# Kernel optimization log

Hardware: AMD Instinct MI355X
Metric: run time of the kernel (lower is better)

## Reference

```python
import jax, jax.numpy as jnp
import numpy as np

ALIGN_WEIGHT = 1.0
UNIFORM_WEIGHT = 1.0
ALIGN_ALPHA = 2.0
UNIFORM_T = 2.0
EPS = 1e-12  # F.normalize eps


def setup_inputs() -> dict:
    key = jax.random.key(0)
    ka, kb = jax.random.split(key)
    B, D = 4096, 256
    return {
        "embeddings_a": jax.random.normal(ka, (B, D), dtype=jnp.float32),
        "embeddings_b": jax.random.normal(kb, (B, D), dtype=jnp.float32),
    }


def _l2_normalize(x):
    # matches F.normalize(p=2, dim=1): x / max(||x||, eps)
    n = jnp.sqrt(jnp.sum(x * x, axis=1, keepdims=True))
    return x / jnp.maximum(n, EPS)


def reference(embeddings_a, embeddings_b):
    a = _l2_normalize(embeddings_a)
    b = _l2_normalize(embeddings_b)

    # alignment: mean ||a_i - b_i||^alpha (alpha=2 -> squared euclidean)
    diff = a - b
    dist = jnp.sqrt(jnp.sum(diff * diff, axis=1))
    align_loss = jnp.mean(dist ** ALIGN_ALPHA)

    # uniformity over concatenated views: mean over strict upper triangle of
    # exp(-t * d_ij^2). Matrix is symmetric with exp(0)=1 on the diagonal, so
    # mean_{i<j} = (sum_all - n) / (n*(n-1)). d^2 = 2 - 2<x_i, x_j> on sphere.
    x = jnp.concatenate([a, b], axis=0)  # [n, d]
    n = x.shape[0]
    gram = x @ x.T                        # [n, n]
    sq = jnp.sum(x * x, axis=1)           # [n]
    d2 = jnp.maximum(sq[:, None] + sq[None, :] - 2.0 * gram, 0.0)
    e = jnp.exp(-UNIFORM_T * d2)
    uniform_loss = (jnp.sum(e) - n) / (n * (n - 1))

    return ALIGN_WEIGHT * align_loss + UNIFORM_WEIGHT * uniform_loss
```

## Files before the change

### kernel.cpp

```cpp
#include <hip/hip_runtime.h>
#include <math.h>

#define D_DIM 256

typedef __attribute__((ext_vector_type(8))) short short8v;
typedef __attribute__((ext_vector_type(16))) float f32x16;

#define AS_GLOBAL(p) ((const __attribute__((address_space(1))) void*)(p))
#define AS_LDS(p)    ((__attribute__((address_space(3))) void*)(p))

__device__ __forceinline__ unsigned short f2bf(float f) {
    unsigned int u = __float_as_uint(f);
    unsigned int r = (u + 0x7fffu + ((u >> 16) & 1u)) >> 16;
    return (unsigned short)r;
}

__global__ __launch_bounds__(256) void normalize_kernel(
        const float* __restrict__ A, const float* __restrict__ Bm,
        unsigned short* __restrict__ Xb, float* __restrict__ SQ,
        float* __restrict__ partials, int B_rows) {
    __shared__ float red[4];
    int lane = threadIdx.x & 63;
    int w    = threadIdx.x >> 6;
    int i    = blockIdx.x * 4 + w;

    const float4* A4 = (const float4*)(A + (size_t)i * D_DIM);
    const float4* B4 = (const float4*)(Bm + (size_t)i * D_DIM);
    float4 av = A4[lane];
    float4 bv = B4[lane];

    float sa = av.x*av.x + av.y*av.y + av.z*av.z + av.w*av.w;
    float sb = bv.x*bv.x + bv.y*bv.y + bv.z*bv.z + bv.w*bv.w;
    #pragma unroll
    for (int off = 32; off > 0; off >>= 1) {
        sa += __shfl_xor(sa, off, 64);
        sb += __shfl_xor(sb, off, 64);
    }
    float dena = fmaxf(sqrtf(sa), 1e-12f);
    float denb = fmaxf(sqrtf(sb), 1e-12f);
    float ia = 1.0f / dena, ib = 1.0f / denb;

    float4 an = {av.x*ia, av.y*ia, av.z*ia, av.w*ia};
    float4 bn = {bv.x*ib, bv.y*ib, bv.z*ib, bv.w*ib};

    ushort4 ua = {f2bf(an.x), f2bf(an.y), f2bf(an.z), f2bf(an.w)};
    ushort4 ub = {f2bf(bn.x), f2bf(bn.y), f2bf(bn.z), f2bf(bn.w)};
    ((ushort4*)(Xb + (size_t)i * D_DIM))[lane]            = ua;
    ((ushort4*)(Xb + (size_t)(B_rows + i) * D_DIM))[lane] = ub;

    float dx = an.x-bn.x, dy = an.y-bn.y, dz = an.z-bn.z, dw = an.w-bn.w;
    float sd = dx*dx + dy*dy + dz*dz + dw*dw;
    #pragma unroll
    for (int off = 32; off > 0; off >>= 1) sd += __shfl_down(sd, off, 64);

    if (lane == 0) {
        SQ[i]          = sa * ia * ia;
        SQ[B_rows + i] = sb * ib * ib;
        red[w] = sd;
    }
    __syncthreads();
    if (threadIdx.x == 0)
        atomicAdd(&partials[blockIdx.x & 63], red[0]+red[1]+red[2]+red[3]);
}

__device__ __forceinline__ short8v frag_read(const unsigned short* base, int r, int kb) {
    int off = r * 128 + (kb ^ ((r & 7) << 4));
    return *reinterpret_cast<const short8v*>(reinterpret_cast<const char*>(base) + off);
}

__global__ __launch_bounds__(256) void uniform_mfma_kernel(
        const unsigned short* __restrict__ Xb, const float* __restrict__ SQ,
        float* __restrict__ partials) {
    int ib = blockIdx.x, jb = blockIdx.y;
    if (jb < ib) return;

    __shared__ __align__(16) unsigned short As[128 * 64];
    __shared__ __align__(16) unsigned short Bs[128 * 64];
    __shared__ float sqa[128], sqb[128], red[4];

    int t    = threadIdx.x;
    int lane = t & 63;
    int w    = t >> 6;
    int wr   = w >> 1, wc = w & 1;

    int rowA0 = ib * 128, rowB0 = jb * 128;
    if (t < 128) sqa[t] = SQ[rowA0 + t];
    else         sqb[t - 128] = SQ[rowB0 + t - 128];

    f32x16 acc[2][2] = {};

    int r_a0 = wr * 64 + (lane & 31), r_a1 = r_a0 + 32;
    int r_b0 = wc * 64 + (lane & 31), r_b1 = r_b0 + 32;

    for (int k0 = 0; k0 < D_DIM; k0 += 64) {
        __syncthreads();
        #pragma unroll
        for (int it = 0; it < 4; ++it) {
            int row   = w * 32 + it * 8 + (lane >> 3);
            int chunk = ((lane & 7) ^ ((lane >> 3) & 7)) << 3;
            const unsigned short* srcA = Xb + (size_t)(rowA0 + row) * D_DIM + k0 + chunk;
            const unsigned short* srcB = Xb + (size_t)(rowB0 + row) * D_DIM + k0 + chunk;
            unsigned short* dA = As + (w * 32 + it * 8) * 64;
            unsigned short* dB = Bs + (w * 32 + it * 8) * 64;
            __builtin_amdgcn_global_load_lds(AS_GLOBAL(srcA), AS_LDS(dA), 16, 0, 0);
            __builtin_amdgcn_global_load_lds(AS_GLOBAL(srcB), AS_LDS(dB), 16, 0, 0);
        }
        __syncthreads();

        #pragma unroll
        for (int kk = 0; kk < 4; ++kk) {
            int kb = kk * 32 + ((lane >> 5) << 4);
            short8v a0 = frag_read(As, r_a0, kb);
            short8v a1 = frag_read(As, r_a1, kb);
            short8v b0 = frag_read(Bs, r_b0, kb);
            short8v b1 = frag_read(Bs, r_b1, kb);
            acc[0][0] = __builtin_amdgcn_mfma_f32_32x32x16_bf16(a0, b0, acc[0][0], 0, 0, 0);
            acc[0][1] = __builtin_amdgcn_mfma_f32_32x32x16_bf16(a0, b1, acc[0][1], 0, 0, 0);
            acc[1][0] = __builtin_amdgcn_mfma_f32_32x32x16_bf16(a1, b0, acc[1][0], 0, 0, 0);
            acc[1][1] = __builtin_amdgcn_mfma_f32_32x32x16_bf16(a1, b1, acc[1][1], 0, 0, 0);
        }
    }

    float s = 0.0f;
    int col = lane & 31;
    int rhi = (lane >> 5) * 4;
    #pragma unroll
    for (int si = 0; si < 2; ++si)
        #pragma unroll
        for (int sj = 0; sj < 2; ++sj)
            #pragma unroll
            for (int reg = 0; reg < 16; ++reg) {
                int il = wr * 64 + si * 32 + (reg & 3) + 8 * (reg >> 2) + rhi;
                int jl = wc * 64 + sj * 32 + col;
                float d2 = fmaxf(sqa[il] + sqb[jl] - 2.0f * acc[si][sj][reg], 0.0f);
                s += __expf(-2.0f * d2);
            }
    if (ib != jb) s *= 2.0f;

    #pragma unroll
    for (int off = 32; off > 0; off >>= 1) s += __shfl_down(s, off, 64);
    if (lane == 0) red[w] = s;
    __syncthreads();
    if (t == 0)
        atomicAdd(&partials[64 + ((ib * 7 + jb * 13) & 63)], red[0]+red[1]+red[2]+red[3]);
}

__global__ void finalize_kernel(const float* __restrict__ partials,
                                float* __restrict__ out, int B_rows) {
    int t = threadIdx.x;
    float al = partials[t];
    float un = partials[64 + t];
    #pragma unroll
    for (int off = 32; off > 0; off >>= 1) {
        al += __shfl_down(al, off, 64);
        un += __shfl_down(un, off, 64);
    }
    if (t == 0) {
        float n = (float)(2 * B_rows);
        out[0] = al / (float)B_rows + (un - n) / (n * (n - 1.0f));
    }
}

extern "C" void kernel_launch(void* const* d_in, const int* in_sizes, int n_in,
                              void* d_out, int out_size, void* d_ws, size_t ws_size,
                              hipStream_t stream) {
    const float* A  = (const float*)d_in[0];
    const float* Bm = (const float*)d_in[1];
    float* out = (float*)d_out;

    int B_rows = in_sizes[0] / D_DIM;
    int n_tot  = 2 * B_rows;

    unsigned short* Xb = (unsigned short*)d_ws;
    float* SQ       = (float*)(Xb + (size_t)n_tot * D_DIM);
    float* partials = SQ + n_tot;

    hipMemsetAsync(partials, 0, 128 * sizeof(float), stream);

    normalize_kernel<<<B_rows / 4, 256, 0, stream>>>(A, Bm, Xb, SQ, partials, B_rows);

    int nb = n_tot / 128;
    uniform_mfma_kernel<<<dim3(nb, nb), 256, 0, stream>>>(Xb, SQ, partials);

    finalize_kernel<<<1, 64, 0, stream>>>(partials, out, B_rows);
}
```

Baseline: 98.38 us.

## Launch triangular grid, switch to 16x16x32 MFMA, drop atomics and memset

```diff
diff --git a/kernel.cpp b/kernel.cpp
--- a/kernel.cpp
+++ b/kernel.cpp
@@ -2,9 +2,12 @@
 #include <math.h>
 
 #define D_DIM 256
+#define TILE  128
+#define BKE   64
+#define LDS_PAD 3072
 
 typedef __attribute__((ext_vector_type(8))) short short8v;
-typedef __attribute__((ext_vector_type(16))) float f32x16;
+typedef __attribute__((ext_vector_type(4))) float f32x4;
 
 #define AS_GLOBAL(p) ((const __attribute__((address_space(1))) void*)(p))
 #define AS_LDS(p)    ((__attribute__((address_space(3))) void*)(p))
@@ -60,79 +63,84 @@
     }
     __syncthreads();
     if (threadIdx.x == 0)
-        atomicAdd(&partials[blockIdx.x & 63], red[0]+red[1]+red[2]+red[3]);
-}
-
-__device__ __forceinline__ short8v frag_read(const unsigned short* base, int r, int kb) {
+        partials[blockIdx.x] = red[0]+red[1]+red[2]+red[3];
+}
+
+__device__ __forceinline__ short8v frag_read(const short* base, int r, int kb) {
     int off = r * 128 + (kb ^ ((r & 7) << 4));
     return *reinterpret_cast<const short8v*>(reinterpret_cast<const char*>(base) + off);
 }
 
-__global__ __launch_bounds__(256) void uniform_mfma_kernel(
+__global__ __launch_bounds__(256, 3) void uniform_mfma_kernel(
         const unsigned short* __restrict__ Xb, const float* __restrict__ SQ,
-        float* __restrict__ partials) {
-    int ib = blockIdx.x, jb = blockIdx.y;
-    if (jb < ib) return;
-
-    __shared__ __align__(16) unsigned short As[128 * 64];
-    __shared__ __align__(16) unsigned short Bs[128 * 64];
-    __shared__ float sqa[128], sqb[128], red[4];
+        float* __restrict__ partials, int n_panels) {
+    __shared__ __align__(16) short As[TILE * BKE + LDS_PAD];
+    __shared__ __align__(16) short Bs[TILE * BKE + LDS_PAD];
+    __shared__ float sqa[TILE], sqb[TILE], red[4];
 
     int t    = threadIdx.x;
     int lane = t & 63;
     int w    = t >> 6;
-    int wr   = w >> 1, wc = w & 1;
-
-    int rowA0 = ib * 128, rowB0 = jb * 128;
-    if (t < 128) sqa[t] = SQ[rowA0 + t];
-    else         sqb[t - 128] = SQ[rowB0 + t - 128];
-
-    f32x16 acc[2][2] = {};
-
-    int r_a0 = wr * 64 + (lane & 31), r_a1 = r_a0 + 32;
-    int r_b0 = wc * 64 + (lane & 31), r_b1 = r_b0 + 32;
-
-    for (int k0 = 0; k0 < D_DIM; k0 += 64) {
+    int wr   = w >> 1;
+    int wc   = w & 1;
+
+    int rem = blockIdx.x;
+    int ib  = 0;
+    while (rem >= n_panels - ib) { rem -= n_panels - ib; ++ib; }
+    int jb = ib + rem;
+
+    int rowA0 = ib * TILE, rowB0 = jb * TILE;
+    if (t < TILE) sqa[t]        = SQ[rowA0 + t];
+    else          sqb[t - TILE] = SQ[rowB0 + t - TILE];
+
+    f32x4 acc[4][4] = {};
+
+    for (int k0 = 0; k0 < D_DIM; k0 += BKE) {
         __syncthreads();
         #pragma unroll
         for (int it = 0; it < 4; ++it) {
-            int row   = w * 32 + it * 8 + (lane >> 3);
-            int chunk = ((lane & 7) ^ ((lane >> 3) & 7)) << 3;
-            const unsigned short* srcA = Xb + (size_t)(rowA0 + row) * D_DIM + k0 + chunk;
-            const unsigned short* srcB = Xb + (size_t)(rowB0 + row) * D_DIM + k0 + chunk;
-            unsigned short* dA = As + (w * 32 + it * 8) * 64;
-            unsigned short* dB = Bs + (w * 32 + it * 8) * 64;
-            __builtin_amdgcn_global_load_lds(AS_GLOBAL(srcA), AS_LDS(dA), 16, 0, 0);
-            __builtin_amdgcn_global_load_lds(AS_GLOBAL(srcB), AS_LDS(dB), 16, 0, 0);
+            int row  = w * 32 + it * 8 + (lane >> 3);
+            int gel  = (((lane & 7) ^ (row & 7)) << 3);
+            const unsigned short* sA = Xb + (size_t)(rowA0 + row) * D_DIM + k0 + gel;
+            const unsigned short* sB = Xb + (size_t)(rowB0 + row) * D_DIM + k0 + gel;
+            short* dA = As + (w * 32 + it * 8) * BKE;
+            short* dB = Bs + (w * 32 + it * 8) * BKE;
+            __builtin_amdgcn_global_load_lds(AS_GLOBAL(sA), AS_LDS(dA), 16, 0, 0);
+            __builtin_amdgcn_global_load_lds(AS_GLOBAL(sB), AS_LDS(dB), 16, 0, 0);
         }
         __syncthreads();
 
         #pragma unroll
-        for (int kk = 0; kk < 4; ++kk) {
-            int kb = kk * 32 + ((lane >> 5) << 4);
-            short8v a0 = frag_read(As, r_a0, kb);
-            short8v a1 = frag_read(As, r_a1, kb);
-            short8v b0 = frag_read(Bs, r_b0, kb);
-            short8v b1 = frag_read(Bs, r_b1, kb);
-            acc[0][0] = __builtin_amdgcn_mfma_f32_32x32x16_bf16(a0, b0, acc[0][0], 0, 0, 0);
-            acc[0][1] = __builtin_amdgcn_mfma_f32_32x32x16_bf16(a0, b1, acc[0][1], 0, 0, 0);
-            acc[1][0] = __builtin_amdgcn_mfma_f32_32x32x16_bf16(a1, b0, acc[1][0], 0, 0, 0);
-            acc[1][1] = __builtin_amdgcn_mfma_f32_32x32x16_bf16(a1, b1, acc[1][1], 0, 0, 0);
+        for (int kk = 0; kk < 2; ++kk) {
+            int kb = kk * 64 + ((lane >> 4) << 4);
+            short8v a[4], b[4];
+            #pragma unroll
+            for (int m = 0; m < 4; ++m)
+                a[m] = frag_read(As, wr * 64 + m * 16 + (lane & 15), kb);
+            #pragma unroll
+            for (int n = 0; n < 4; ++n)
+                b[n] = frag_read(Bs, wc * 64 + n * 16 + (lane & 15), kb);
+            #pragma unroll
+            for (int m = 0; m < 4; ++m)
+                #pragma unroll
+                for (int n = 0; n < 4; ++n)
+                    acc[m][n] = __builtin_amdgcn_mfma_f32_16x16x32_bf16(
+                        a[m], b[n], acc[m][n], 0, 0, 0);
         }
     }
 
-    float s = 0.0f;
-    int col = lane & 31;
-    int rhi = (lane >> 5) * 4;
-    #pragma unroll
-    for (int si = 0; si < 2; ++si)
+    float s   = 0.0f;
+    int   col = lane & 15;
+    int   rhi = (lane >> 4) * 4;
+    #pragma unroll
+    for (int m = 0; m < 4; ++m)
         #pragma unroll
-        for (int sj = 0; sj < 2; ++sj)
-            #pragma unroll
-            for (int reg = 0; reg < 16; ++reg) {
-                int il = wr * 64 + si * 32 + (reg & 3) + 8 * (reg >> 2) + rhi;
-                int jl = wc * 64 + sj * 32 + col;
-                float d2 = fmaxf(sqa[il] + sqb[jl] - 2.0f * acc[si][sj][reg], 0.0f);
+        for (int n = 0; n < 4; ++n)
+            #pragma unroll
+            for (int reg = 0; reg < 4; ++reg) {
+                int il = wr * 64 + m * 16 + rhi + reg;
+                int jl = wc * 64 + n * 16 + col;
+                float d2 = fmaxf(sqa[il] + sqb[jl] - 2.0f * acc[m][n][reg], 0.0f);
                 s += __expf(-2.0f * d2);
             }
     if (ib != jb) s *= 2.0f;
@@ -142,22 +150,29 @@
     if (lane == 0) red[w] = s;
     __syncthreads();
     if (t == 0)
-        atomicAdd(&partials[64 + ((ib * 7 + jb * 13) & 63)], red[0]+red[1]+red[2]+red[3]);
-}
-
-__global__ void finalize_kernel(const float* __restrict__ partials,
-                                float* __restrict__ out, int B_rows) {
+        partials[1024 + blockIdx.x] = red[0]+red[1]+red[2]+red[3];
+}
+
+__global__ __launch_bounds__(256) void finalize_kernel(
+        const float* __restrict__ partials, float* __restrict__ out,
+        int B_rows, int n_blocks) {
+    __shared__ float reda[4], redu[4];
     int t = threadIdx.x;
-    float al = partials[t];
-    float un = partials[64 + t];
+    float al = 0.0f, un = 0.0f;
+    for (int i = t; i < 1024; i += 256)      al += partials[i];
+    for (int i = t; i < n_blocks; i += 256)  un += partials[1024 + i];
     #pragma unroll
     for (int off = 32; off > 0; off >>= 1) {
         al += __shfl_down(al, off, 64);
         un += __shfl_down(un, off, 64);
     }
+    if ((t & 63) == 0) { reda[t >> 6] = al; redu[t >> 6] = un; }
+    __syncthreads();
     if (t == 0) {
+        float sal = reda[0]+reda[1]+reda[2]+reda[3];
+        float sun = redu[0]+redu[1]+redu[2]+redu[3];
         float n = (float)(2 * B_rows);
-        out[0] = al / (float)B_rows + (un - n) / (n * (n - 1.0f));
+        out[0] = sal / (float)B_rows + (sun - n) / (n * (n - 1.0f));
     }
 }
 
@@ -175,12 +190,11 @@
     float* SQ       = (float*)(Xb + (size_t)n_tot * D_DIM);
     float* partials = SQ + n_tot;
 
-    hipMemsetAsync(partials, 0, 128 * sizeof(float), stream);
-
     normalize_kernel<<<B_rows / 4, 256, 0, stream>>>(A, Bm, Xb, SQ, partials, B_rows);
 
-    int nb = n_tot / 128;
-    uniform_mfma_kernel<<<dim3(nb, nb), 256, 0, stream>>>(Xb, SQ, partials);
-
-    finalize_kernel<<<1, 64, 0, stream>>>(partials, out, B_rows);
-}
+    int n_panels = n_tot / TILE;
+    int n_blocks = n_panels * (n_panels + 1) / 2;
+    uniform_mfma_kernel<<<n_blocks, 256, 0, stream>>>(Xb, SQ, partials, n_panels);
+
+    finalize_kernel<<<1, 256, 0, stream>>>(partials, out, B_rows, n_blocks);
+}
```

Measured after the change: 88.36 us. -10.2%, faster.
